# Performance work log

Measured on AMD Instinct MI355X. Metric: run time of the kernel, lower is better.

The kernel has to match this reference:

```python
import jax, jax.numpy as jnp
import numpy as np


def _blended_linear(h, W, b, blend):
    # Equivalent to building w[b] = sum_e blend[e,b]*W[e] (shape B,out,in)
    # and computing w[b] @ h[b] + sum_e blend[e,b]*b[e], without the huge
    # per-sample weight tensor.
    # h: (B, in), W: (E, out, in), b: (E, out), blend: (E, B) -> (B, out)
    y = jnp.einsum('eoi,bi->ebo', W, h)          # per-expert outputs
    y = jnp.einsum('eb,ebo->bo', blend, y)       # blend across experts
    return y + blend.T @ b                       # blended bias


def setup_inputs() -> dict:
    key = jax.random.key(0)
    ks = jax.random.split(key, 9)
    E, B = 8, 8192
    dims = [480, 512, 512, 363]
    inp = {
        'x': jax.random.normal(ks[0], (B, dims[0]), jnp.float32),
        'weight_blend': jax.random.uniform(ks[1], (E, B), jnp.float32),
        'W1': jax.random.normal(ks[2], (E, dims[1], dims[0]), jnp.float32) * 0.05,
        'b1': jax.random.normal(ks[3], (E, dims[1]), jnp.float32) * 0.05,
        'W2': jax.random.normal(ks[4], (E, dims[2], dims[1]), jnp.float32) * 0.05,
        'b2': jax.random.normal(ks[5], (E, dims[2]), jnp.float32) * 0.05,
        'W3': jax.random.normal(ks[6], (E, dims[3], dims[2]), jnp.float32) * 0.05,
        'b3': jax.random.normal(ks[7], (E, dims[3]), jnp.float32) * 0.05,
        'batch_size': B,
    }
    return inp


def reference(x, weight_blend, W1, b1, W2, b2, W3, b3, batch_size):
    # Dropout layers are identity in eval mode; final_ac=True -> softmax.
    h = _blended_linear(x, W1, b1, weight_blend)
    h = jax.nn.elu(h)
    h = _blended_linear(h, W2, b2, weight_blend)
    h = jax.nn.elu(h)
    h = _blended_linear(h, W3, b3, weight_blend)
    return jax.nn.softmax(h, axis=-1)
```

## Files before the change

kernel.cpp:

```cpp
#include <hip/hip_runtime.h>
#include <cstdint>

#define E_EXP 8
#define BATCH 8192
#define D0 480
#define D1 512
#define D2 512
#define D3 363
#define KP 512
#define N3PAD 384

typedef _Float16 f16x8 __attribute__((ext_vector_type(8)));
typedef float f32x16 __attribute__((ext_vector_type(16)));
typedef unsigned short u16;

__device__ __forceinline__ u16 f2h(float f) {
    _Float16 h = (_Float16)f;
    return __builtin_bit_cast(u16, h);
}

__device__ __forceinline__ void async16(const u16* g, u16* s) {
    __builtin_amdgcn_global_load_lds(
        reinterpret_cast<const __attribute__((address_space(1))) void*>(
            reinterpret_cast<uintptr_t>(g)),
        reinterpret_cast<__attribute__((address_space(3))) void*>(
            reinterpret_cast<uintptr_t>(s)),
        16, 0, 0);
}

__device__ __forceinline__ void pack_seg(const float* __restrict__ src,
                                         u16* __restrict__ dst,
                                         int OUT_src, int OUTP, int IN_src) {
    int total = E_EXP * OUTP * 128;
    int in4 = IN_src >> 2;
    for (int idx = blockIdx.x * blockDim.x + threadIdx.x; idx < total;
         idx += gridDim.x * blockDim.x) {
        int e = idx / (OUTP * 128);
        int r = idx - e * OUTP * 128;
        int o = r >> 7;
        int k4 = r & 127;
        ushort4 w;
        if (o < OUT_src && k4 < in4) {
            const float4 v = *reinterpret_cast<const float4*>(
                src + ((size_t)e * OUT_src + o) * IN_src + (k4 << 2));
            w.x = f2h(v.x); w.y = f2h(v.y); w.z = f2h(v.z); w.w = f2h(v.w);
        } else {
            w.x = 0; w.y = 0; w.z = 0; w.w = 0;
        }
        *reinterpret_cast<ushort4*>(dst + ((size_t)e * OUTP + o) * KP + (k4 << 2)) = w;
    }
}

__global__ void pack_all(const float* __restrict__ W1, const float* __restrict__ W2,
                         const float* __restrict__ W3, u16* __restrict__ wf1,
                         u16* __restrict__ wf2, u16* __restrict__ wf3) {
    pack_seg(W1, wf1, 512, 512, D0);
    pack_seg(W2, wf2, 512, 512, D1);
    pack_seg(W3, wf3, D3, N3PAD, D2);
}

__global__ void pad_x(const float* __restrict__ x, u16* __restrict__ xp) {
    int total = BATCH * 128;
    for (int idx = blockIdx.x * blockDim.x + threadIdx.x; idx < total;
         idx += gridDim.x * blockDim.x) {
        int b = idx >> 7, k4 = idx & 127;
        ushort4 w;
        if (k4 < 120) {
            const float4 v = *reinterpret_cast<const float4*>(
                x + (size_t)b * D0 + (k4 << 2));
            w.x = f2h(v.x); w.y = f2h(v.y); w.z = f2h(v.z); w.w = f2h(v.w);
        } else {
            w.x = 0; w.y = 0; w.z = 0; w.w = 0;
        }
        *reinterpret_cast<ushort4*>(xp + (size_t)b * KP + (k4 << 2)) = w;
    }
}

__global__ __launch_bounds__(512, 2) void gemm_all(
    const u16* __restrict__ A, const u16* __restrict__ Bw,
    const float* __restrict__ blend, const float* __restrict__ bias,
    u16* __restrict__ out, int OUTP, int OUTR, int nbn, int mode) {
    __shared__ __align__(16) u16 S[49152];
    const int tid = threadIdx.x;
    const int w = tid >> 6, lane = tid & 63;
    const int wm2 = w & 3, wn2 = w >> 2;
    const int l31 = lane & 31, q2 = lane >> 5;

    const int id = blockIdx.x;
    const int xcd = id & 7;
    const int j = id >> 3;
    const int bm = ((j & 3) << 3) + xcd;
    const int bn = j >> 2;

    f32x16 acc[2][2];
#pragma unroll
    for (int mg = 0; mg < 2; ++mg)
#pragma unroll
        for (int kk = 0; kk < 2; ++kk)
#pragma unroll
            for (int i = 0; i < 16; ++i) acc[mg][kk][i] = 0.f;

    _Float16 blh[8][2];
#pragma unroll
    for (int e = 0; e < 8; ++e)
#pragma unroll
        for (int mg = 0; mg < 2; ++mg)
            blh[e][mg] = (_Float16)blend[e * BATCH + bm * 256 + wm2 * 64 +
                                         mg * 32 + l31];

    const int l4r = lane >> 2;
    const int l4s = lane & 3;
    const int ks8 = (l4s ^ ((l4r >> 1) & 3)) << 3;
    const size_t EST = (size_t)OUTP * KP;
    const u16* gA0 = A + (size_t)(bm * 256 + w * 32 + l4r) * KP + ks8;
    const u16* gB0 = Bw + (size_t)w * EST + (size_t)(bn * 64 + l4r) * KP + ks8;
    const size_t R16 = (size_t)16 * KP;
    const int aBase = w * 1024;
    const int bBase = 8192 + w * 2048;

    int aoff[2][2], boff[2];
#pragma unroll
    for (int mg = 0; mg < 2; ++mg) {
        int r = wm2 * 64 + mg * 32 + l31;
        int base = (r >> 4) * 512 + (r & 15) * 32;
        int swz = (r >> 1) & 3;
#pragma unroll
        for (int kk = 0; kk < 2; ++kk)
            aoff[mg][kk] = base + (((kk * 2 + q2) ^ swz) << 3);
    }
    {
        int r = wn2 * 32 + l31;
        int base = (r >> 4) * 512 + (r & 15) * 32;
        int swz = (r >> 1) & 3;
#pragma unroll
        for (int kk = 0; kk < 2; ++kk)
            boff[kk] = base + (((kk * 2 + q2) ^ swz) << 3);
    }

    auto stage = [&](int kt, int p) {
        const int ko = kt << 5;
        u16* buf = S + p * 24576;
        async16(gA0 + ko, buf + aBase);
        async16(gA0 + R16 + ko, buf + aBase + 512);
        async16(gB0 + ko, buf + bBase);
        async16(gB0 + R16 + ko, buf + bBase + 512);
        async16(gB0 + 2 * R16 + ko, buf + bBase + 1024);
        async16(gB0 + 3 * R16 + ko, buf + bBase + 1536);
    };

    stage(0, 0);
    __syncthreads();

#pragma unroll 2
    for (int kt = 0; kt < 16; ++kt) {
        const int p = kt & 1;
        if (kt < 15) stage(kt + 1, p ^ 1);
        const u16* As_ = S + p * 24576;
        const u16* Bs_ = As_ + 8192;
        f16x8 af[2][2];
#pragma unroll
        for (int mg = 0; mg < 2; ++mg)
#pragma unroll
            for (int kk = 0; kk < 2; ++kk)
                af[mg][kk] = *reinterpret_cast<const f16x8*>(&As_[aoff[mg][kk]]);
#pragma unroll
        for (int e = 0; e < 8; ++e) {
            f16x8 bf0 = *reinterpret_cast<const f16x8*>(&Bs_[e * 2048 + boff[0]]);
            f16x8 bf1 = *reinterpret_cast<const f16x8*>(&Bs_[e * 2048 + boff[1]]);
#pragma unroll
            for (int mg = 0; mg < 2; ++mg) {
                f16x8 a0 = af[mg][0] * blh[e][mg];
                acc[mg][0] = __builtin_amdgcn_mfma_f32_32x32x16_f16(
                    a0, bf0, acc[mg][0], 0, 0, 0);
                f16x8 a1 = af[mg][1] * blh[e][mg];
                acc[mg][1] = __builtin_amdgcn_mfma_f32_32x32x16_f16(
                    a1, bf1, acc[mg][1], 0, 0, 0);
            }
        }
        __syncthreads();
    }

    float* Blf = reinterpret_cast<float*>(S);
    float* Bif = reinterpret_cast<float*>(S + 8192);
    for (int idx = tid; idx < 2048; idx += 512) {
        int e = idx >> 8, r = idx & 255;
        Blf[r * 9 + e] = blend[e * BATCH + bm * 256 + r];
    }
    {
        int e = tid >> 6, c = tid & 63;
        int cg = bn * 64 + c;
        Bif[c * 9 + e] = (cg < OUTR) ? bias[e * OUTR + cg] : 0.f;
    }
    __syncthreads();

    const int col_l = wn2 * 32 + l31;
    const int gcol = bn * 64 + col_l;
    float bif[8];
#pragma unroll
    for (int e = 0; e < 8; ++e) bif[e] = Bif[col_l * 9 + e];
#pragma unroll
    for (int mg = 0; mg < 2; ++mg) {
#pragma unroll
        for (int reg = 0; reg < 16; ++reg) {
            int rloc = (reg & 3) + ((reg >> 2) << 3) + (q2 << 2);
            int rl = wm2 * 64 + mg * 32 + rloc;
            float bb = 0.f;
#pragma unroll
            for (int e = 0; e < 8; ++e) bb += Blf[rl * 9 + e] * bif[e];
            float v = acc[mg][0][reg] + acc[mg][1][reg] + bb;
            if (mode == 0) v = v > 0.f ? v : expm1f(v);
            out[(size_t)(bm * 256 + rl) * OUTP + gcol] = f2h(v);
        }
    }
}

__global__ __launch_bounds__(128) void softmax_rows(
    const u16* __restrict__ P, float* __restrict__ out) {
    const int b = blockIdx.x;
    const int tid = threadIdx.x, lane = tid & 63, w = tid >> 6;
    float v[3];
    int n = 0;
    float mx = -3.4e38f;
    for (int i = tid; i < D3; i += 128) {
        float s = (float)*reinterpret_cast<const _Float16*>(
            P + (size_t)b * N3PAD + i);
        v[n] = s; mx = fmaxf(mx, s); ++n;
    }
#pragma unroll
    for (int off = 32; off >= 1; off >>= 1) mx = fmaxf(mx, __shfl_xor(mx, off, 64));
    __shared__ float sm[4];
    if (lane == 0) sm[w] = mx;
    __syncthreads();
    mx = fmaxf(sm[0], sm[1]);
    float s = 0.f;
    for (int jj = 0; jj < n; ++jj) { v[jj] = expf(v[jj] - mx); s += v[jj]; }
#pragma unroll
    for (int off = 32; off >= 1; off >>= 1) s += __shfl_xor(s, off, 64);
    if (lane == 0) sm[2 + w] = s;
    __syncthreads();
    float inv = 1.f / (sm[2] + sm[3]);
    n = 0;
    for (int i = tid; i < D3; i += 128) { out[(size_t)b * D3 + i] = v[n] * inv; ++n; }
}

extern "C" void kernel_launch(void* const* d_in, const int* in_sizes, int n_in,
                              void* d_out, int out_size, void* d_ws, size_t ws_size,
                              hipStream_t stream) {
    const float* x = (const float*)d_in[0];
    const float* blend = (const float*)d_in[1];
    const float* W1 = (const float*)d_in[2];
    const float* b1 = (const float*)d_in[3];
    const float* W2 = (const float*)d_in[4];
    const float* b2 = (const float*)d_in[5];
    const float* W3 = (const float*)d_in[6];
    const float* b3 = (const float*)d_in[7];
    float* outp = (float*)d_out;

    char* ws = (char*)d_ws;
    u16* wf1 = (u16*)ws; ws += (size_t)E_EXP * 512 * KP * 2;
    u16* wf2 = (u16*)ws; ws += (size_t)E_EXP * 512 * KP * 2;
    u16* wf3 = (u16*)ws; ws += (size_t)E_EXP * N3PAD * KP * 2;
    u16* xp = (u16*)ws;  ws += (size_t)BATCH * KP * 2;
    u16* h1 = (u16*)ws;  ws += (size_t)BATCH * KP * 2;
    u16* h2 = (u16*)ws;  ws += (size_t)BATCH * KP * 2;
    u16* P = (u16*)ws;

    pack_all<<<1024, 256, 0, stream>>>(W1, W2, W3, wf1, wf2, wf3);
    pad_x<<<2048, 256, 0, stream>>>(x, xp);

    gemm_all<<<32 * 8, 512, 0, stream>>>(xp, wf1, blend, b1, h1, 512, 512, 8, 0);
    gemm_all<<<32 * 8, 512, 0, stream>>>(h1, wf2, blend, b2, h2, 512, 512, 8, 0);
    gemm_all<<<32 * 6, 512, 0, stream>>>(h2, wf3, blend, b3, P, N3PAD, D3, 6, 1);
    softmax_rows<<<BATCH, 128, 0, stream>>>(P, outp);
}
```

Measured before the change: 217.4 us.

## Halve GEMM M-tile to 128 rows with 256-thread blocks and raise MFMA priority

The blended GEMM kernel drops from 256-row tiles with 8 waves to 128-row tiles with 4 waves, so each wave now stages two experts' B tiles. This doubles the grid to 512 or 384 blocks, filling the 256 CUs more evenly and cutting LDS per block. It also wraps the MFMA loop in s_setprio to favour compute issue. The tradeoff is that B weights get re-read from global/L2 twice as often, because each weight tile now serves half as many rows.

```diff
diff --git a/kernel.cpp b/kernel.cpp
--- a/kernel.cpp
+++ b/kernel.cpp
@@ -76,21 +76,21 @@
     }
 }
 
-__global__ __launch_bounds__(512, 2) void gemm_all(
+__global__ __launch_bounds__(256, 2) void gemm_all(
     const u16* __restrict__ A, const u16* __restrict__ Bw,
     const float* __restrict__ blend, const float* __restrict__ bias,
     u16* __restrict__ out, int OUTP, int OUTR, int nbn, int mode) {
-    __shared__ __align__(16) u16 S[49152];
+    __shared__ __align__(16) u16 S[40960];
     const int tid = threadIdx.x;
     const int w = tid >> 6, lane = tid & 63;
-    const int wm2 = w & 3, wn2 = w >> 2;
+    const int wm = w & 1, wn = w >> 1;
     const int l31 = lane & 31, q2 = lane >> 5;
 
     const int id = blockIdx.x;
     const int xcd = id & 7;
     const int j = id >> 3;
-    const int bm = ((j & 3) << 3) + xcd;
-    const int bn = j >> 2;
+    const int bm = ((j & 7) << 3) + xcd;
+    const int bn = j >> 3;
 
     f32x16 acc[2][2];
 #pragma unroll
@@ -105,23 +105,25 @@
     for (int e = 0; e < 8; ++e)
 #pragma unroll
         for (int mg = 0; mg < 2; ++mg)
-            blh[e][mg] = (_Float16)blend[e * BATCH + bm * 256 + wm2 * 64 +
+            blh[e][mg] = (_Float16)blend[e * BATCH + bm * 128 + wm * 64 +
                                          mg * 32 + l31];
 
     const int l4r = lane >> 2;
     const int l4s = lane & 3;
     const int ks8 = (l4s ^ ((l4r >> 1) & 3)) << 3;
     const size_t EST = (size_t)OUTP * KP;
-    const u16* gA0 = A + (size_t)(bm * 256 + w * 32 + l4r) * KP + ks8;
-    const u16* gB0 = Bw + (size_t)w * EST + (size_t)(bn * 64 + l4r) * KP + ks8;
+    const u16* gA0 = A + (size_t)(bm * 128 + w * 32 + l4r) * KP + ks8;
+    const u16* gB0 = Bw + (size_t)(2 * w) * EST + (size_t)(bn * 64 + l4r) * KP + ks8;
+    const u16* gB1 = gB0 + EST;
     const size_t R16 = (size_t)16 * KP;
     const int aBase = w * 1024;
-    const int bBase = 8192 + w * 2048;
+    const int bBase0 = 4096 + (2 * w) * 2048;
+    const int bBase1 = bBase0 + 2048;
 
     int aoff[2][2], boff[2];
 #pragma unroll
     for (int mg = 0; mg < 2; ++mg) {
-        int r = wm2 * 64 + mg * 32 + l31;
+        int r = wm * 64 + mg * 32 + l31;
         int base = (r >> 4) * 512 + (r & 15) * 32;
         int swz = (r >> 1) & 3;
 #pragma unroll
@@ -129,7 +131,7 @@
             aoff[mg][kk] = base + (((kk * 2 + q2) ^ swz) << 3);
     }
     {
-        int r = wn2 * 32 + l31;
+        int r = wn * 32 + l31;
         int base = (r >> 4) * 512 + (r & 15) * 32;
         int swz = (r >> 1) & 3;
 #pragma unroll
@@ -139,13 +141,14 @@
 
     auto stage = [&](int kt, int p) {
         const int ko = kt << 5;
-        u16* buf = S + p * 24576;
+        u16* buf = S + p * 20480;
         async16(gA0 + ko, buf + aBase);
         async16(gA0 + R16 + ko, buf + aBase + 512);
-        async16(gB0 + ko, buf + bBase);
-        async16(gB0 + R16 + ko, buf + bBase + 512);
-        async16(gB0 + 2 * R16 + ko, buf + bBase + 1024);
-        async16(gB0 + 3 * R16 + ko, buf + bBase + 1536);
+#pragma unroll
+        for (int c = 0; c < 4; ++c) {
+            async16(gB0 + c * R16 + ko, buf + bBase0 + c * 512);
+            async16(gB1 + c * R16 + ko, buf + bBase1 + c * 512);
+        }
     };
 
     stage(0, 0);
@@ -155,14 +158,15 @@
     for (int kt = 0; kt < 16; ++kt) {
         const int p = kt & 1;
         if (kt < 15) stage(kt + 1, p ^ 1);
-        const u16* As_ = S + p * 24576;
-        const u16* Bs_ = As_ + 8192;
+        const u16* As_ = S + p * 20480;
+        const u16* Bs_ = As_ + 4096;
         f16x8 af[2][2];
 #pragma unroll
         for (int mg = 0; mg < 2; ++mg)
 #pragma unroll
             for (int kk = 0; kk < 2; ++kk)
                 af[mg][kk] = *reinterpret_cast<const f16x8*>(&As_[aoff[mg][kk]]);
+        __builtin_amdgcn_s_setprio(1);
 #pragma unroll
         for (int e = 0; e < 8; ++e) {
             f16x8 bf0 = *reinterpret_cast<const f16x8*>(&Bs_[e * 2048 + boff[0]]);
@@ -177,23 +181,24 @@
                     a1, bf1, acc[mg][1], 0, 0, 0);
             }
         }
+        __builtin_amdgcn_s_setprio(0);
         __syncthreads();
     }
 
     float* Blf = reinterpret_cast<float*>(S);
     float* Bif = reinterpret_cast<float*>(S + 8192);
-    for (int idx = tid; idx < 2048; idx += 512) {
-        int e = idx >> 8, r = idx & 255;
-        Blf[r * 9 + e] = blend[e * BATCH + bm * 256 + r];
-    }
-    {
-        int e = tid >> 6, c = tid & 63;
+    for (int idx = tid; idx < 1024; idx += 256) {
+        int e = idx >> 7, r = idx & 127;
+        Blf[r * 9 + e] = blend[e * BATCH + bm * 128 + r];
+    }
+    for (int idx = tid; idx < 512; idx += 256) {
+        int e = idx >> 6, c = idx & 63;
         int cg = bn * 64 + c;
         Bif[c * 9 + e] = (cg < OUTR) ? bias[e * OUTR + cg] : 0.f;
     }
     __syncthreads();
 
-    const int col_l = wn2 * 32 + l31;
+    const int col_l = wn * 32 + l31;
     const int gcol = bn * 64 + col_l;
     float bif[8];
 #pragma unroll
@@ -203,13 +208,13 @@
 #pragma unroll
         for (int reg = 0; reg < 16; ++reg) {
             int rloc = (reg & 3) + ((reg >> 2) << 3) + (q2 << 2);
-            int rl = wm2 * 64 + mg * 32 + rloc;
+            int rl = wm * 64 + mg * 32 + rloc;
             float bb = 0.f;
 #pragma unroll
             for (int e = 0; e < 8; ++e) bb += Blf[rl * 9 + e] * bif[e];
             float v = acc[mg][0][reg] + acc[mg][1][reg] + bb;
             if (mode == 0) v = v > 0.f ? v : expm1f(v);
-            out[(size_t)(bm * 256 + rl) * OUTP + gcol] = f2h(v);
+            out[(size_t)(bm * 128 + rl) * OUTP + gcol] = f2h(v);
         }
     }
 }
@@ -268,8 +273,8 @@
     pack_all<<<1024, 256, 0, stream>>>(W1, W2, W3, wf1, wf2, wf3);
     pad_x<<<2048, 256, 0, stream>>>(x, xp);
 
-    gemm_all<<<32 * 8, 512, 0, stream>>>(xp, wf1, blend, b1, h1, 512, 512, 8, 0);
-    gemm_all<<<32 * 8, 512, 0, stream>>>(h1, wf2, blend, b2, h2, 512, 512, 8, 0);
-    gemm_all<<<32 * 6, 512, 0, stream>>>(h2, wf3, blend, b3, P, N3PAD, D3, 6, 1);
+    gemm_all<<<64 * 8, 256, 0, stream>>>(xp, wf1, blend, b1, h1, 512, 512, 8, 0);
+    gemm_all<<<64 * 8, 256, 0, stream>>>(h1, wf2, blend, b2, h2, 512, 512, 8, 0);
+    gemm_all<<<64 * 6, 256, 0, stream>>>(h2, wf3, blend, b3, P, N3PAD, D3, 6, 1);
     softmax_rows<<<BATCH, 128, 0, stream>>>(P, outp);
 }
```

After: 227.3 us. 1.05x slower.
